# Kernel tuning notes

Hardware: AMD Instinct MI355X
Metric: run time of the kernel (lower is better)

## Reference

```python
import jax, jax.numpy as jnp
import numpy as np

N_HEADS = 16


def setup_inputs() -> dict:
    key = jax.random.key(0)
    k1, k2 = jax.random.split(key)
    B, S, D = 2, 2048, 2048
    x = jax.random.normal(k1, (B, S, D), dtype=jnp.float32)
    # torch nn.Linear(dim, 3*dim): y = x @ W^T + b; store W in jax layout [D, 3D]
    W_qkv = jax.random.normal(k2, (D, 3 * D), dtype=jnp.float32) * (D ** -0.5)
    b_qkv = jnp.zeros((3 * D,), dtype=jnp.float32)
    mask = jnp.ones((B, S), dtype=bool)
    return {"x": x, "W_qkv": W_qkv, "b_qkv": b_qkv, "mask": mask}


def reference(x, W_qkv, b_qkv, mask):
    B, S, D = x.shape
    H = N_HEADS
    hd = D // H
    scale = hd ** -0.5
    qkv = x @ W_qkv + b_qkv                      # [B,S,3D]
    q, k, v = jnp.split(qkv, 3, axis=-1)
    # [B,S,D] -> [B,H,S,hd]
    reshape = lambda t: t.reshape(B, S, H, hd).transpose(0, 2, 1, 3)
    q, k, v = reshape(q), reshape(k), reshape(v)
    sim = jnp.einsum('bhqd,bhkd->bhqk', q, k) * scale   # [B,H,S,S]
    neg = -jnp.finfo(sim.dtype).max
    sim = jnp.where(mask[:, None, None, :], sim, neg)   # padding mask on keys
    attn = jax.nn.softmax(sim, axis=-1)
    out = jnp.einsum('bhqk,bhkd->bhqd', attn, v)        # [B,H,S,hd]
    return out.transpose(0, 2, 1, 3).reshape(B, S, D)
```

## Files before the change

kernel.cpp:

```cpp
#include <hip/hip_runtime.h>
#include <hip/hip_bf16.h>
#include <math.h>

typedef __attribute__((ext_vector_type(8))) short bf16x8;
typedef __attribute__((ext_vector_type(4))) float f32x4;
typedef __attribute__((ext_vector_type(16))) float f32x16;
typedef __attribute__((ext_vector_type(4))) short short4v;
typedef __attribute__((ext_vector_type(4))) int int4v;
typedef __attribute__((ext_vector_type(4))) unsigned uint4v;

__device__ __forceinline__ short f2bf(float f) {
  union { float f; unsigned u; } v; v.f = f;
  unsigned r = v.u + 0x7fffu + ((v.u >> 16) & 1u);
  return (short)(r >> 16);
}

__device__ __forceinline__ unsigned cvt_pk_bf16(float lo, float hi) {
  unsigned r;
  asm volatile("v_cvt_pk_bf16_f32 %0, %1, %2" : "=v"(r) : "v"(lo), "v"(hi));
  return r;
}


__global__ void convert_x_kernel(const float* __restrict__ x, short* __restrict__ xb, int n) {
  int i = (blockIdx.x * blockDim.x + threadIdx.x) * 4;
  int stride = gridDim.x * blockDim.x * 4;
  for (; i < n; i += stride) {
    float4 v = *(const float4*)(x + i);
    short4v o;
    o.x = f2bf(v.x); o.y = f2bf(v.y); o.z = f2bf(v.z); o.w = f2bf(v.w);
    *(short4v*)(xb + i) = o;
  }
}

__global__ void transpose_w_kernel(const float* __restrict__ W, short* __restrict__ Wt) {
  __shared__ short tile[32][33];
  int n0 = blockIdx.x * 32, k0 = blockIdx.y * 32;
  int tx = threadIdx.x, ty = threadIdx.y;
#pragma unroll
  for (int u = 0; u < 4; ++u) {
    int k = k0 + ty + u * 8;
    tile[ty + u * 8][tx] = f2bf(W[(size_t)k * 6144 + n0 + tx]);
  }
  __syncthreads();
#pragma unroll
  for (int u = 0; u < 4; ++u) {
    int n = n0 + ty + u * 8;
    Wt[(size_t)n * 2048 + k0 + tx] = tile[tx][ty + u * 8];
  }
}

__global__ void mask_norm_kernel(const unsigned* __restrict__ m, unsigned char* __restrict__ out, int n) {
  __shared__ int flagA, flagB;
  if (threadIdx.x == 0) { flagA = 0; flagB = 0; }
  __syncthreads();
  int a = 0, b = 0;
  for (int i = threadIdx.x; i < n / 4; i += blockDim.x) {
    unsigned wv = m[i];
    if (wv > 1u) a = 1;
    if (wv != 0u && wv != 0x3f800000u) b = 1;
  }
  if (a) atomicOr(&flagA, 1);
  if (b) atomicOr(&flagB, 1);
  __syncthreads();
  int A = flagA, B = flagB;
  for (int i = threadIdx.x; i < n; i += blockDim.x) {
    unsigned char r;
    if (!A) r = (m[i] != 0u) ? 1 : 0;
    else if (!B) r = (((const float*)m)[i] != 0.f) ? 1 : 0;
    else r = (((const unsigned char*)m)[i] != 0) ? 1 : 0;
    out[i] = r;
  }
}


__global__ __launch_bounds__(512, 2) void qkv_gemm_kernel(
    const short* __restrict__ A, const short* __restrict__ Bt, const float* __restrict__ bias,
    short* __restrict__ qws, short* __restrict__ kws, short* __restrict__ vtws) {
  __shared__ __align__(16) char smem[131072];

  int lid = blockIdx.x;
  int swz = (lid & 7) * 48 + (lid >> 3);
  int tm = swz / 24, tn = swz % 24;
  int m0 = tm * 256, n0 = tn * 256;
  int t = threadIdx.x, lane = t & 63, w = t >> 6;
  int wr = w >> 2, wc = w & 3;
  int g = lane >> 4, c = lane & 15;

#define AHP(P, hm) (smem + (P) * 65536 + (hm) * 16384)
#define BHP(P, hn) (smem + (P) * 65536 + 32768 + (hn) * 16384)

#define STAGE_HALF(ldsb, gbase)                                                            \
  { _Pragma("unroll")                                                                      \
    for (int rr = 0; rr < 2; ++rr) {                                                       \
      int ci = rr * 512 + t;                                                               \
      int row_ = ci >> 3, ch_ = ci & 7;                                                    \
      const short* gp_ = (gbase) + (size_t)row_ * 2048 + ((ch_ ^ (row_ & 7)) * 8);         \
      __builtin_amdgcn_global_load_lds((const __attribute__((address_space(1))) void*)gp_, \
          (__attribute__((address_space(3))) void*)((ldsb) + ci * 16), 16, 0, 0);          \
    } }

#define LD_A(half)                                                                          \
  { const char* ab_ = AHP(P, half);                                                         \
    _Pragma("unroll")                                                                       \
    for (int mi = 0; mi < 4; ++mi) {                                                        \
      int row_ = wr * 16 + c + mi * 32;                                                     \
      _Pragma("unroll")                                                                     \
      for (int ks = 0; ks < 2; ++ks)                                                        \
        af[mi][ks] = *(const bf16x8*)(ab_ + row_ * 128 + (((ks * 4 + g) ^ (row_ & 7)) * 16)); \
    } }
#define LD_B(half)                                                                          \
  { const char* bb_ = BHP(P, half);                                                         \
    _Pragma("unroll")                                                                       \
    for (int nj = 0; nj < 2; ++nj) {                                                        \
      int row_ = wc * 16 + c + nj * 64;                                                     \
      _Pragma("unroll")                                                                     \
      for (int ks = 0; ks < 2; ++ks)                                                        \
        bfr[nj][ks] = *(const bf16x8*)(bb_ + row_ * 128 + (((ks * 4 + g) ^ (row_ & 7)) * 16)); \
    } }
#define MFMA16(MI0, NJ0)                                                                    \
  __builtin_amdgcn_s_setprio(1);                                                            \
  _Pragma("unroll")                                                                         \
  for (int mi = 0; mi < 4; ++mi)                                                            \
    _Pragma("unroll")                                                                       \
    for (int nj = 0; nj < 2; ++nj)                                                          \
      _Pragma("unroll")                                                                     \
      for (int ks = 0; ks < 2; ++ks)                                                        \
        acc[(MI0) + mi][(NJ0) + nj] =                                                       \
            __builtin_amdgcn_mfma_f32_16x16x32_bf16(af[mi][ks], bfr[nj][ks],                \
                                                    acc[(MI0) + mi][(NJ0) + nj], 0, 0, 0);  \
  __builtin_amdgcn_s_setprio(0);

  STAGE_HALF(AHP(0, 0), A + (size_t)m0 * 2048);
  STAGE_HALF(BHP(0, 0), Bt + (size_t)n0 * 2048);
  STAGE_HALF(BHP(0, 1), Bt + (size_t)(n0 + 128) * 2048);
  STAGE_HALF(AHP(0, 1), A + (size_t)(m0 + 128) * 2048);
  asm volatile("s_waitcnt vmcnt(4)" ::: "memory");
  __builtin_amdgcn_s_barrier();

  f32x4 acc[8][4] = {};

  for (int tk = 0; tk < 32; ++tk) {
    int P = tk & 1, Pn = P ^ 1;
    bool pf = (tk + 1 < 32);
    int k1 = (tk + 1) * 64;
    bf16x8 af[4][2], bfr[2][2];

    LD_A(0); LD_B(0);
    if (pf) STAGE_HALF(AHP(Pn, 0), A + (size_t)m0 * 2048 + k1);
    MFMA16(0, 0);
    if (pf) { asm volatile("s_waitcnt vmcnt(4)" ::: "memory"); }
    else    { asm volatile("s_waitcnt vmcnt(2)" ::: "memory"); }
    __builtin_amdgcn_s_barrier();

    LD_B(1);
    if (pf) STAGE_HALF(BHP(Pn, 0), Bt + (size_t)n0 * 2048 + k1);
    MFMA16(0, 2);
    if (pf) { asm volatile("s_waitcnt vmcnt(4)" ::: "memory"); }
    else    { asm volatile("s_waitcnt vmcnt(0)" ::: "memory"); }
    __builtin_amdgcn_s_barrier();

    LD_A(1);
    if (pf) STAGE_HALF(BHP(Pn, 1), Bt + (size_t)(n0 + 128) * 2048 + k1);
    MFMA16(4, 2);
    __builtin_amdgcn_s_barrier();

    LD_B(0);
    if (pf) STAGE_HALF(AHP(Pn, 1), A + (size_t)(m0 + 128) * 2048 + k1);
    MFMA16(4, 0);
    if (pf) { asm volatile("s_waitcnt vmcnt(4)" ::: "memory"); }
    __builtin_amdgcn_s_barrier();
  }

  int sec = n0 >> 11;
  int b = m0 >> 11;
  int s0 = m0 & 2047;
  int nsec = n0 & 2047;

  if (sec < 2) {
    short* base = (sec == 0 ? qws : kws);
    const float scq = (sec == 0) ? (0.08838834764831845f * 1.4426950408889634f) : 1.0f;
#pragma unroll
    for (int nj = 0; nj < 4; ++nj) {
      int colsec = nsec + wc * 16 + nj * 64;
      float bv = bias[n0 + wc * 16 + nj * 64 + c];
      int h = colsec >> 7;
      int d = (colsec & 127) + c;
      short* dst = base + ((size_t)(b * 16 + h)) * (2048 * 128) + d;
#pragma unroll
      for (int mi = 0; mi < 8; ++mi) {
        int srow = s0 + (wr + 2 * mi) * 16 + g * 4;
#pragma unroll
        for (int r = 0; r < 4; ++r)
          dst[(size_t)(srow + r) * 128] = f2bf((acc[mi][nj][r] + bv) * scq);
      }
    }
  } else {
    __builtin_amdgcn_s_barrier();
    char* wreg = smem + w * 16384;
#pragma unroll
    for (int nj = 0; nj < 4; ++nj) {
      float bv = bias[n0 + wc * 16 + nj * 64 + c];
      int d = nj * 16 + c;
#pragma unroll
      for (int mi = 0; mi < 8; ++mi)
#pragma unroll
        for (int r = 0; r < 4; ++r) {
          int sloc = mi * 16 + g * 4 + r;
          *(short*)(wreg + d * 256 + (((sloc >> 3) ^ (d & 15)) * 16) + (sloc & 7) * 2) =
              f2bf(acc[mi][nj][r] + bv);
        }
    }
#pragma unroll
    for (int q = 0; q < 16; ++q) {
      int d = q * 4 + g;
      bf16x8 v = *(const bf16x8*)(wreg + d * 256 + ((c ^ (d & 15)) * 16));
      int colsec = nsec + wc * 16 + (d >> 4) * 64 + (d & 15);
      int h = colsec >> 7, dloc = colsec & 127;
      int srow = s0 + wr * 16 + (c >> 1) * 32 + (c & 1) * 8;
      *(bf16x8*)(vtws + ((size_t)(b * 16 + h)) * (128 * 2048) + (size_t)dloc * 2048 + srow) = v;
    }
  }
#undef AHP
#undef BHP
#undef STAGE_HALF
#undef LD_A
#undef LD_B
#undef MFMA16
}


__global__ __launch_bounds__(256, 2) void attn_kernel(
    const short* __restrict__ qws, const short* __restrict__ kws, const short* __restrict__ vtws,
    const unsigned char* __restrict__ maskb, float* __restrict__ out) {
  __shared__ short Ks[2][32 * 128];
  __shared__ short Vs[2][128 * 32];
  __shared__ float biasLds[2048];
  __shared__ int flagsLds[64];

  const int S = 2048, HD = 128;
  int lid = blockIdx.x;
  int swz = (lid & 7) * 64 + (lid >> 3);
  int bh = swz >> 4, qblk = swz & 15;
  int b = bh >> 4, h = bh & 15;
  int t = threadIdx.x, lane = t & 63, w = t >> 6;
  int ql = lane & 31, hi = lane >> 5;
  int q0 = qblk * 128 + w * 32;
  const short* Q = qws + (size_t)bh * S * HD;
  const short* Kp = kws + (size_t)bh * S * HD;
  const short* Vt = vtws + (size_t)bh * HD * S;
  const unsigned char* mk = maskb + b * S;
  const float NEG = -3.4028235e38f;

#define STAGE_KV(buf, kv0_)                                                              \
  {                                                                                      \
    _Pragma("unroll")                                                                    \
    for (int rr = 0; rr < 2; ++rr) {                                                     \
      int ci = rr * 256 + t;                                                             \
      int r = ci >> 4, cin = ci & 15;                                                    \
      const short* gk = Kp + (size_t)((kv0_) + r) * HD + ((cin ^ (r & 7)) * 8);          \
      __builtin_amdgcn_global_load_lds((const __attribute__((address_space(1))) void*)gk,\
          (__attribute__((address_space(3))) void*)(&Ks[buf][0] + ci * 8), 16, 0, 0);    \
    }                                                                                    \
    _Pragma("unroll")                                                                    \
    for (int rr = 0; rr < 2; ++rr) {                                                     \
      int ci = rr * 256 + t;                                                             \
      int r = ci >> 2, cin = ci & 3;                                                     \
      const short* gv = Vt + (size_t)r * S + (kv0_) + ((cin ^ ((r >> 1) & 3)) * 8);      \
      __builtin_amdgcn_global_load_lds((const __attribute__((address_space(1))) void*)gv,\
          (__attribute__((address_space(3))) void*)(&Vs[buf][0] + ci * 8), 16, 0, 0);    \
    }                                                                                    \
  }

#define QK_PHASE(CUR)                                                                    \
  { const short* ks = &Ks[CUR][0];                                                       \
    _Pragma("unroll") for (int r = 0; r < 16; ++r) sv[r] = 0.f;                          \
    __builtin_amdgcn_s_setprio(1);                                                       \
    _Pragma("unroll") for (int kc = 0; kc < 8; ++kc) {                                   \
      int chunk = (kc * 2 + hi) ^ (ql & 7);                                              \
      bf16x8 kf = *(const bf16x8*)(ks + ql * 128 + chunk * 8);                           \
      sv = __builtin_amdgcn_mfma_f32_32x32x16_bf16(kf, qf[kc], sv, 0, 0, 0);             \
    }                                                                                    \
    __builtin_amdgcn_s_setprio(0); }

#define PV_PHASE()                                                                       \
  { __builtin_amdgcn_s_setprio(1);                                                       \
    _Pragma("unroll") for (int dt = 0; dt < 4; ++dt)                                     \
      _Pragma("unroll") for (int kt = 0; kt < 2; ++kt)                                   \
        acc[dt] = __builtin_amdgcn_mfma_f32_32x32x16_bf16(vreg[dt * 2 + kt], pfv[kt],    \
                                                          acc[dt], 0, 0, 0);             \
    __builtin_amdgcn_s_setprio(0); }

#define LOADV(CUR)                                                                       \
  { const short* vs = &Vs[CUR][0];                                                       \
    _Pragma("unroll") for (int dt = 0; dt < 4; ++dt)                                     \
      _Pragma("unroll") for (int kt = 0; kt < 2; ++kt) {                                 \
        int d = dt * 32 + ql;                                                            \
        int chunk = (kt * 2 + hi) ^ ((d >> 1) & 3);                                      \
        vreg[dt * 2 + kt] = *(const bf16x8*)(vs + d * 32 + chunk * 8);                   \
      } }

#define SOFTMAX_PACK(IT_)                                                                \
  { int kv0s = (IT_) * 32;                                                               \
    float p[16];                                                                         \
    if ((fmask >> (IT_)) & 1ull) {                                                       \
      _Pragma("unroll") for (int r = 0; r < 16; ++r) p[r] = sv[r];                       \
    } else {                                                                             \
      _Pragma("unroll") for (int g2 = 0; g2 < 4; ++g2) {                                 \
        f32x4 bb = *(const f32x4*)(biasLds + kv0s + g2 * 8 + hi * 4);                    \
        _Pragma("unroll") for (int j = 0; j < 4; ++j)                                    \
          p[g2 * 4 + j] = sv[g2 * 4 + j] + bb[j];                                        \
      }                                                                                  \
    }                                                                                    \
    float a0 = fmaxf(fmaxf(p[0], p[1]), fmaxf(p[2], p[3]));                              \
    float a1 = fmaxf(fmaxf(p[4], p[5]), fmaxf(p[6], p[7]));                              \
    float a2 = fmaxf(fmaxf(p[8], p[9]), fmaxf(p[10], p[11]));                            \
    float a3 = fmaxf(fmaxf(p[12], p[13]), fmaxf(p[14], p[15]));                          \
    float rmx = fmaxf(fmaxf(a0, a1), fmaxf(a2, a3));                                     \
    rmx = fmaxf(rmx, __shfl_xor(rmx, 32));                                               \
    if (__any(rmx > m_ + 12.f)) {                                                        \
      float mn = fmaxf(m_, rmx);                                                         \
      float al = exp2f(m_ - mn);                                                         \
      m_ = mn; lp *= al;                                                                 \
      _Pragma("unroll") for (int dt = 0; dt < 4; ++dt)                                   \
        _Pragma("unroll") for (int r = 0; r < 16; ++r) acc[dt][r] *= al;                 \
    }                                                                                    \
    _Pragma("unroll") for (int r = 0; r < 16; ++r) p[r] = exp2f(p[r] - m_);              \
    lp += (((p[0] + p[1]) + (p[2] + p[3])) + ((p[4] + p[5]) + (p[6] + p[7])))            \
        + (((p[8] + p[9]) + (p[10] + p[11])) + ((p[12] + p[13]) + (p[14] + p[15])));     \
    _Pragma("unroll") for (int kt = 0; kt < 2; ++kt) {                                   \
      unsigned Aw = cvt_pk_bf16(p[kt * 8 + 0], p[kt * 8 + 1]);                           \
      unsigned Bw = cvt_pk_bf16(p[kt * 8 + 2], p[kt * 8 + 3]);                           \
      unsigned Cw = cvt_pk_bf16(p[kt * 8 + 4], p[kt * 8 + 5]);                           \
      unsigned Dw = cvt_pk_bf16(p[kt * 8 + 6], p[kt * 8 + 7]);                           \
      asm volatile("v_permlane32_swap_b32 %0, %1" : "+v"(Aw), "+v"(Cw));                 \
      asm volatile("v_permlane32_swap_b32 %0, %1" : "+v"(Bw), "+v"(Dw));                 \
      uint4v uu; uu.x = Aw; uu.y = Bw; uu.z = Cw; uu.w = Dw;                             \
      pfv[kt] = __builtin_bit_cast(bf16x8, uu);                                          \
    } }

  bf16x8 qf[8];
#pragma unroll
  for (int kc = 0; kc < 8; ++kc)
    qf[kc] = *(const bf16x8*)(Q + (size_t)(q0 + ql) * HD + kc * 16 + hi * 8);

  for (int i = t; i < 2048; i += 256) biasLds[i] = mk[i] ? 0.f : NEG;
  STAGE_KV(0, 0);
  __syncthreads();
  if (t < 64) {
    int ok = 1;
    for (int j = 0; j < 32; ++j) ok &= (biasLds[t * 32 + j] == 0.f) ? 1 : 0;
    flagsLds[t] = ok;
  }
  __syncthreads();
  unsigned long long fmask = __ballot(flagsLds[lane] != 0);

  f32x16 acc[4] = {};
  float m_ = NEG, lp = 0.f;
  f32x16 sv;
  bf16x8 pfv[2];
  bf16x8 vreg[8];

  QK_PHASE(0);
  STAGE_KV(1, 32);
  SOFTMAX_PACK(0);
  LOADV(0);
  __syncthreads();

  for (int it = 1; it < 64; ++it) {
    int cur = it & 1;
    QK_PHASE(cur);
    if (it < 63) STAGE_KV(cur ^ 1, it * 32 + 32);
    PV_PHASE();
    LOADV(cur);
    SOFTMAX_PACK(it);
    __syncthreads();
  }
  PV_PHASE();

  lp += __shfl_xor(lp, 32);
  float inv = 1.f / lp;
  size_t orow = (size_t)(b * 2048 + q0 + ql) * 2048 + h * 128;
#pragma unroll
  for (int dt = 0; dt < 4; ++dt)
#pragma unroll
    for (int g2 = 0; g2 < 4; ++g2) {
      f32x4 v;
      v[0] = acc[dt][g2 * 4 + 0] * inv;
      v[1] = acc[dt][g2 * 4 + 1] * inv;
      v[2] = acc[dt][g2 * 4 + 2] * inv;
      v[3] = acc[dt][g2 * 4 + 3] * inv;
      int d = dt * 32 + g2 * 8 + hi * 4;
      *(f32x4*)(out + orow + d) = v;
    }
#undef STAGE_KV
#undef QK_PHASE
#undef PV_PHASE
#undef LOADV
#undef SOFTMAX_PACK
}


extern "C" void kernel_launch(void* const* d_in, const int* in_sizes, int n_in,
                              void* d_out, int out_size, void* d_ws, size_t ws_size,
                              hipStream_t stream) {
  const float* x = (const float*)d_in[0];
  const float* W = (const float*)d_in[1];
  const float* bias = (const float*)d_in[2];
  const void* mask = d_in[3];
  float* out = (float*)d_out;

  char* ws = (char*)d_ws;
  short* xb = (short*)(ws);
  short* wt = (short*)(ws + 16777216);
  short* qws = (short*)(ws + 41943040);
  short* kws = (short*)(ws + 58720256);
  short* vtws = (short*)(ws + 75497472);
  unsigned char* maskb = (unsigned char*)(ws + 92274688);

  convert_x_kernel<<<dim3(2048), dim3(256), 0, stream>>>(x, xb, 2 * 2048 * 2048);
  transpose_w_kernel<<<dim3(192, 64), dim3(32, 8), 0, stream>>>(W, wt);
  mask_norm_kernel<<<dim3(1), dim3(256), 0, stream>>>((const unsigned*)mask, maskb, 2 * 2048);
  qkv_gemm_kernel<<<dim3(384), dim3(512), 0, stream>>>(xb, wt, bias, qws, kws, vtws);
  attn_kernel<<<dim3(512), dim3(256), 0, stream>>>(qws, kws, vtws, maskb, out);
}
```

Before: 334.9 us.

## Deepen QKV GEMM LDS pipeline with rotating 16KB slots and extra prefetch

```diff
diff --git a/kernel.cpp b/kernel.cpp
--- a/kernel.cpp
+++ b/kernel.cpp
@@ -87,21 +87,20 @@
   int wr = w >> 2, wc = w & 3;
   int g = lane >> 4, c = lane & 15;
 
-#define AHP(P, hm) (smem + (P) * 65536 + (hm) * 16384)
-#define BHP(P, hn) (smem + (P) * 65536 + 32768 + (hn) * 16384)
-
-#define STAGE_HALF(ldsb, gbase)                                                            \
+#define SLOT(s) (smem + (s) * 16384)
+
+#define STAGE(s, gbase)                                                                    \
   { _Pragma("unroll")                                                                      \
     for (int rr = 0; rr < 2; ++rr) {                                                       \
       int ci = rr * 512 + t;                                                               \
       int row_ = ci >> 3, ch_ = ci & 7;                                                    \
       const short* gp_ = (gbase) + (size_t)row_ * 2048 + ((ch_ ^ (row_ & 7)) * 8);         \
       __builtin_amdgcn_global_load_lds((const __attribute__((address_space(1))) void*)gp_, \
-          (__attribute__((address_space(3))) void*)((ldsb) + ci * 16), 16, 0, 0);          \
+          (__attribute__((address_space(3))) void*)(SLOT(s) + ci * 16), 16, 0, 0);         \
     } }
 
-#define LD_A(half)                                                                          \
-  { const char* ab_ = AHP(P, half);                                                         \
+#define LD_A(s)                                                                             \
+  { const char* ab_ = SLOT(s);                                                              \
     _Pragma("unroll")                                                                       \
     for (int mi = 0; mi < 4; ++mi) {                                                        \
       int row_ = wr * 16 + c + mi * 32;                                                     \
@@ -109,16 +108,16 @@
       for (int ks = 0; ks < 2; ++ks)                                                        \
         af[mi][ks] = *(const bf16x8*)(ab_ + row_ * 128 + (((ks * 4 + g) ^ (row_ & 7)) * 16)); \
     } }
-#define LD_B(half)                                                                          \
-  { const char* bb_ = BHP(P, half);                                                         \
+#define LD_B(s, R)                                                                          \
+  { const char* bb_ = SLOT(s);                                                              \
     _Pragma("unroll")                                                                       \
     for (int nj = 0; nj < 2; ++nj) {                                                        \
       int row_ = wc * 16 + c + nj * 64;                                                     \
       _Pragma("unroll")                                                                     \
       for (int ks = 0; ks < 2; ++ks)                                                        \
-        bfr[nj][ks] = *(const bf16x8*)(bb_ + row_ * 128 + (((ks * 4 + g) ^ (row_ & 7)) * 16)); \
+        R[nj][ks] = *(const bf16x8*)(bb_ + row_ * 128 + (((ks * 4 + g) ^ (row_ & 7)) * 16)); \
     } }
-#define MFMA16(MI0, NJ0)                                                                    \
+#define MFMA16(MI0, NJ0, BF)                                                                \
   __builtin_amdgcn_s_setprio(1);                                                            \
   _Pragma("unroll")                                                                         \
   for (int mi = 0; mi < 4; ++mi)                                                            \
@@ -127,49 +126,69 @@
       _Pragma("unroll")                                                                     \
       for (int ks = 0; ks < 2; ++ks)                                                        \
         acc[(MI0) + mi][(NJ0) + nj] =                                                       \
-            __builtin_amdgcn_mfma_f32_16x16x32_bf16(af[mi][ks], bfr[nj][ks],                \
+            __builtin_amdgcn_mfma_f32_16x16x32_bf16(af[mi][ks], BF[nj][ks],                 \
                                                     acc[(MI0) + mi][(NJ0) + nj], 0, 0, 0);  \
   __builtin_amdgcn_s_setprio(0);
 
-  STAGE_HALF(AHP(0, 0), A + (size_t)m0 * 2048);
-  STAGE_HALF(BHP(0, 0), Bt + (size_t)n0 * 2048);
-  STAGE_HALF(BHP(0, 1), Bt + (size_t)(n0 + 128) * 2048);
-  STAGE_HALF(AHP(0, 1), A + (size_t)(m0 + 128) * 2048);
-  asm volatile("s_waitcnt vmcnt(4)" ::: "memory");
-  __builtin_amdgcn_s_barrier();
+#define BAR() __builtin_amdgcn_s_barrier()
+#define VMC(N) asm volatile("s_waitcnt vmcnt(" #N ")" ::: "memory")
+
+  const short* Ab0 = A + (size_t)m0 * 2048;
+  const short* Ab1 = A + (size_t)(m0 + 128) * 2048;
+  const short* Bb0 = Bt + (size_t)n0 * 2048;
+  const short* Bb1 = Bt + (size_t)(n0 + 128) * 2048;
 
   f32x4 acc[8][4] = {};
-
-  for (int tk = 0; tk < 32; ++tk) {
-    int P = tk & 1, Pn = P ^ 1;
-    bool pf = (tk + 1 < 32);
-    int k1 = (tk + 1) * 64;
-    bf16x8 af[4][2], bfr[2][2];
-
-    LD_A(0); LD_B(0);
-    if (pf) STAGE_HALF(AHP(Pn, 0), A + (size_t)m0 * 2048 + k1);
-    MFMA16(0, 0);
-    if (pf) { asm volatile("s_waitcnt vmcnt(4)" ::: "memory"); }
-    else    { asm volatile("s_waitcnt vmcnt(2)" ::: "memory"); }
-    __builtin_amdgcn_s_barrier();
-
-    LD_B(1);
-    if (pf) STAGE_HALF(BHP(Pn, 0), Bt + (size_t)n0 * 2048 + k1);
-    MFMA16(0, 2);
-    if (pf) { asm volatile("s_waitcnt vmcnt(4)" ::: "memory"); }
-    else    { asm volatile("s_waitcnt vmcnt(0)" ::: "memory"); }
-    __builtin_amdgcn_s_barrier();
-
-    LD_A(1);
-    if (pf) STAGE_HALF(BHP(Pn, 1), Bt + (size_t)(n0 + 128) * 2048 + k1);
-    MFMA16(4, 2);
-    __builtin_amdgcn_s_barrier();
-
-    LD_B(0);
-    if (pf) STAGE_HALF(AHP(Pn, 1), A + (size_t)(m0 + 128) * 2048 + k1);
-    MFMA16(4, 0);
-    if (pf) { asm volatile("s_waitcnt vmcnt(4)" ::: "memory"); }
-    __builtin_amdgcn_s_barrier();
+  bf16x8 af[4][2], b0r[2][2], b1r[2][2];
+
+  STAGE(0, Ab0); STAGE(1, Bb0); STAGE(2, Bb1); STAGE(3, Ab1);
+  STAGE(4, Ab0 + 64); STAGE(5, Bb0 + 64);
+  VMC(8);
+  BAR();
+
+  for (int tk = 0; tk < 30; ++tk) {
+    int P2 = (tk & 1) * 4, Q2 = P2 ^ 4;
+    int kb = tk * 64;
+    LD_A(P2 + 0); LD_B(P2 + 1, b0r);
+    STAGE(Q2 + 2, Bb1 + kb + 64);
+    BAR();
+    MFMA16(0, 0, b0r);
+    VMC(6); BAR();
+    LD_B(P2 + 2, b1r);
+    STAGE(Q2 + 3, Ab1 + kb + 64);
+    BAR();
+    MFMA16(0, 2, b1r);
+    VMC(6); BAR();
+    LD_A(P2 + 3);
+    STAGE(P2 + 0, Ab0 + kb + 128);
+    BAR();
+    MFMA16(4, 2, b1r);
+    VMC(6); BAR();
+    STAGE(P2 + 1, Bb0 + kb + 128);
+    BAR();
+    MFMA16(4, 0, b0r);
+    VMC(6); BAR();
+  }
+
+  {
+    LD_A(0); LD_B(1, b0r);
+    STAGE(6, Bb1 + 1984);
+    BAR(); MFMA16(0, 0, b0r); VMC(6); BAR();
+    LD_B(2, b1r);
+    STAGE(7, Ab1 + 1984);
+    BAR(); MFMA16(0, 2, b1r); VMC(6); BAR();
+    LD_A(3);
+    BAR(); MFMA16(4, 2, b1r); VMC(6); BAR();
+    BAR(); MFMA16(4, 0, b0r); VMC(4); BAR();
+  }
+  {
+    LD_A(4); LD_B(5, b0r);
+    BAR(); MFMA16(0, 0, b0r); VMC(2); BAR();
+    LD_B(6, b1r);
+    BAR(); MFMA16(0, 2, b1r); VMC(0); BAR();
+    LD_A(7);
+    BAR(); MFMA16(4, 2, b1r); BAR();
+    BAR(); MFMA16(4, 0, b0r); BAR();
   }
 
   int sec = n0 >> 11;
@@ -221,12 +240,13 @@
       *(bf16x8*)(vtws + ((size_t)(b * 16 + h)) * (128 * 2048) + (size_t)dloc * 2048 + srow) = v;
     }
   }
-#undef AHP
-#undef BHP
-#undef STAGE_HALF
+#undef SLOT
+#undef STAGE
 #undef LD_A
 #undef LD_B
 #undef MFMA16
+#undef BAR
+#undef VMC
 }
 
 
```

Result: no change. 337.6 us (+0.8%).
